# Kernel tuning notes

Hardware: AMD Instinct MI355X
Metric: run time of the kernel (lower is better)

Reference implementation:

```python
import jax, jax.numpy as jnp
import numpy as np

N = 50000
E = 400000
IN_NODE = 256
IN_EATTR = 64
IN_ETYPE = 64
EMB_EATTR = 128
EMB_ETYPE = 128
EMB_NODE = 128
OUT = 128
HEADS = 8
N_NODE_TYPES = 3
SLOPE = 0.2


def _lrelu(x):
    return jnp.where(x >= 0, x, SLOPE * x)


def setup_inputs() -> dict:
    key = jax.random.key(0)
    ks = jax.random.split(key, 12)
    s = lambda fan_in: 1.0 / np.sqrt(fan_in)
    return {
        "node_feats": jax.random.normal(ks[0], (N, IN_NODE), dtype=jnp.float32),
        "edge_index": jax.random.randint(ks[1], (2, E), 0, N, dtype=jnp.int64),
        "edge_attr": jax.random.normal(ks[2], (E, IN_EATTR), dtype=jnp.float32),
        "edge_type": jax.random.normal(ks[3], (E, IN_ETYPE), dtype=jnp.float32),
        "node_type_list": jax.random.randint(ks[4], (N,), 0, N_NODE_TYPES, dtype=jnp.int64),
        "edge_type_list": jax.random.randint(ks[5], (E,), 0, 4, dtype=jnp.int64),
        # one Linear per node type, stacked: [T, in, emb]
        "W_node": jax.random.uniform(ks[6], (N_NODE_TYPES, IN_NODE, EMB_NODE), jnp.float32, -s(IN_NODE), s(IN_NODE)),
        "W_eattr": jax.random.uniform(ks[7], (IN_EATTR, EMB_EATTR), jnp.float32, -s(IN_EATTR), s(IN_EATTR)),
        "W_etype": jax.random.uniform(ks[8], (IN_ETYPE, EMB_ETYPE), jnp.float32, -s(IN_ETYPE), s(IN_ETYPE)),
        "W_upd": jax.random.uniform(ks[9], (EMB_NODE + EMB_EATTR, OUT), jnp.float32, -s(EMB_NODE + EMB_EATTR), s(EMB_NODE + EMB_EATTR)),
        "W_attn": jax.random.uniform(ks[10], (EMB_EATTR + EMB_ETYPE + 2 * EMB_NODE, HEADS), jnp.float32, -s(512), s(512)),
    }


def reference(node_feats, edge_index, edge_attr, edge_type, node_type_list,
              edge_type_list, W_node, W_eattr, W_etype, W_upd, W_attn):
    # type-specific node embedding: project with all type weights, select per node
    all_emb = jnp.einsum("ni,tio->tno", node_feats, W_node)            # [T, N, emb]
    node_emb = jnp.take_along_axis(all_emb, node_type_list[None, :, None], axis=0)[0]  # [N, emb]

    attr_emb = _lrelu(edge_attr @ W_eattr)                             # [E, emb_a]
    type_emb = _lrelu(edge_type @ W_etype)                             # [E, emb_t]

    src, tar = edge_index[0], edge_index[1]
    src_emb = node_emb[src]                                            # [E, emb]
    tar_emb = node_emb[tar]                                            # [E, emb]

    # cat(tar_emb, attr_emb, type_emb, src_emb) -> attention scores per edge
    feat = jnp.concatenate([tar_emb, attr_emb, type_emb, src_emb], axis=1)
    scores = _lrelu(feat @ W_attn)                                     # [E, H]

    # segment softmax over edges grouped by SOURCE node (torch softmax(dim=1)
    # on the dense [src, tar, H] matrix; -10000 fillers underflow to 0)
    seg_max = jax.ops.segment_max(scores, src, num_segments=N)         # [N, H]
    ex = jnp.exp(scores - seg_max[src])
    denom = jax.ops.segment_sum(ex, src, num_segments=N)               # [N, H]
    attn = ex / denom[src]                                             # [E, H]

    msg = _lrelu(jnp.concatenate([src_emb, attr_emb], axis=1) @ W_upd) # [E, O]
    out = jax.ops.segment_sum(attn[:, :, None] * msg[:, None, :], src, num_segments=N)  # [N, H, O]
    return out.reshape(N, HEADS * OUT)
```

## Files before the change

kernel.cpp:

```cpp
#include <hip/hip_runtime.h>
#include <hip/hip_bf16.h>

#define N_NODES 50000
#define N_EDGES 400000
#define SLOPE 0.2f

typedef __attribute__((ext_vector_type(8))) short bf16x8;
typedef __attribute__((ext_vector_type(4))) float f32x4;
#define MFMA_BF16 __builtin_amdgcn_mfma_f32_16x16x32_bf16

static __device__ __forceinline__ float lrelu(float x) { return x >= 0.f ? x : SLOPE * x; }
static __device__ __forceinline__ float b2f(__hip_bfloat16 x) { return __bfloat162float(x); }
static __device__ __forceinline__ float u2f(unsigned short u) {
    union { unsigned short u; __hip_bfloat16 b; } cv; cv.u = u; return __bfloat162float(cv.b);
}
static __device__ __forceinline__ unsigned short f2bf(float x) {
    union { __hip_bfloat16 b; unsigned short u; } cv; cv.b = __float2bfloat16(x); return cv.u;
}
static __device__ __forceinline__ int clampi(int v, int lo, int hi) {
    return v < lo ? lo : (v > hi ? hi : v);
}
static __device__ __forceinline__ float ldF(const void* __restrict__ p, size_t i, bool isb) {
    return isb ? b2f(((const __hip_bfloat16*)p)[i]) : ((const float*)p)[i];
}
static __device__ __forceinline__ int ldI(const void* __restrict__ p, size_t i, bool i64) {
    return i64 ? (int)(((const long long*)p)[i]) : ((const int*)p)[i];
}

__global__ void k_detect(const void* __restrict__ nf, const void* __restrict__ eidx,
                         int* __restrict__ flags)
{
    int t = threadIdx.x;
    float x = b2f(((const __hip_bfloat16*)nf)[2 * t]);
    bool bad = !(x == x) || fabsf(x) > 1e4f;
    unsigned long long fmask = __ballot(bad);
    int v = ((const int*)eidx)[2 * t + 1];
    unsigned long long imask = __ballot(v != 0);
    if (t == 0) {
        flags[0] = (fmask == 0ull) ? 1 : 0;
        flags[1] = (imask == 0ull) ? 1 : 0;
    }
}

__global__ __launch_bounds__(256) void k_wprep(
    const void* __restrict__ Wn, const void* __restrict__ Wea, const void* __restrict__ Wet,
    const void* __restrict__ Wup, const void* __restrict__ Wat,
    unsigned short* __restrict__ WnT, unsigned short* __restrict__ WeaT,
    unsigned short* __restrict__ WetT, unsigned short* __restrict__ Wu1T,
    unsigned short* __restrict__ Wu2T, unsigned short* __restrict__ WatMidT,
    unsigned short* __restrict__ WatTS, const int* __restrict__ flags)
{
    const bool isb = flags[0] != 0;
    int i = blockIdx.x * 256 + threadIdx.x;
    if (i < 3 * 128 * 256) {
        int ty = i >> 15, rem = i & 32767, c = rem >> 8, k = rem & 255;
        WnT[i] = f2bf(ldF(Wn, ((size_t)ty * 256 + k) * 128 + c, isb));
    }
    if (i < 128 * 128) {
        int c = i >> 7, k = i & 127;
        Wu1T[i] = f2bf(ldF(Wup, (size_t)k * 128 + c, isb));
        Wu2T[i] = f2bf(ldF(Wup, (size_t)(128 + k) * 128 + c, isb));
    }
    if (i < 128 * 64) {
        int c = i >> 6, k = i & 63;
        WeaT[i] = f2bf(ldF(Wea, (size_t)k * 128 + c, isb));
        WetT[i] = f2bf(ldF(Wet, (size_t)k * 128 + c, isb));
    }
    if (i < 16 * 256) {
        int c = i >> 8, k = i & 255;
        WatMidT[i] = (c < 8) ? f2bf(ldF(Wat, (size_t)(128 + k) * 8 + c, isb)) : (unsigned short)0;
    }
    if (i < 16 * 128) {
        int c = i >> 7, k = i & 127;
        WatTS[i] = (c < 8) ? f2bf(ldF(Wat, (size_t)k * 8 + c, isb))
                           : f2bf(ldF(Wat, (size_t)(384 + k) * 8 + (c - 8), isb));
    }
}

__global__ __launch_bounds__(256) void k_node(
    const void* __restrict__ nf, const void* __restrict__ ntype,
    const unsigned short* __restrict__ WnT, const unsigned short* __restrict__ Wu1T,
    const unsigned short* __restrict__ WatTS,
    unsigned short* __restrict__ base, float* __restrict__ c_ts,
    const int* __restrict__ flags)
{
    const bool isb = flags[0] != 0, i64 = flags[1] != 0;
    const int t = threadIdx.x, lane = t & 63, wid = t >> 6;
    const int m = wid & 1, nh = wid >> 1;
    const int lr = lane & 15, lg = lane >> 4;
    const int n0 = blockIdx.x * 32;

    __shared__ __align__(16) unsigned short s_x[32 * 264];
    __shared__ __align__(16) unsigned short s_emb[32 * 136];
    __shared__ int s_ty[32];

    if (t < 32) {
        int nn = n0 + t;
        s_ty[t] = clampi(ldI(ntype, nn < N_NODES ? nn : N_NODES - 1, i64), 0, 2);
    }
    if (isb) {
        for (int i = t; i < 32 * 32; i += 256) {
            int r = i >> 5, c8 = (i & 31) * 8;
            bf16x8 v = (bf16x8)(short)0;
            if (n0 + r < N_NODES)
                v = *(const bf16x8*)((const unsigned short*)nf + (size_t)(n0 + r) * 256 + c8);
            *(bf16x8*)&s_x[r * 264 + c8] = v;
        }
    } else {
        for (int i = t; i < 32 * 64; i += 256) {
            int r = i >> 6, c4 = (i & 63) * 4;
            float4 v = make_float4(0.f, 0.f, 0.f, 0.f);
            if (n0 + r < N_NODES)
                v = *(const float4*)((const float*)nf + (size_t)(n0 + r) * 256 + c4);
            unsigned short* d = &s_x[r * 264 + c4];
            d[0] = f2bf(v.x); d[1] = f2bf(v.y); d[2] = f2bf(v.z); d[3] = f2bf(v.w);
        }
    }
    __syncthreads();

    bf16x8 A[8];
    #pragma unroll
    for (int ks = 0; ks < 8; ++ks)
        A[ks] = *(const bf16x8*)&s_x[(m * 16 + lr) * 264 + ks * 32 + lg * 8];

    f32x4 acc0[4], acc1[4], acc2[4];
    #pragma unroll
    for (int ct = 0; ct < 4; ++ct) {
        acc0[ct] = (f32x4)(0.f); acc1[ct] = (f32x4)(0.f); acc2[ct] = (f32x4)(0.f);
    }
    #pragma unroll
    for (int ct = 0; ct < 4; ++ct) {
        const int crow = nh * 64 + ct * 16 + lr;
        #pragma unroll
        for (int ks = 0; ks < 8; ++ks) {
            const int koff = ks * 32 + lg * 8;
            bf16x8 B0 = *(const bf16x8*)(WnT + (size_t)crow * 256 + koff);
            bf16x8 B1 = *(const bf16x8*)(WnT + (size_t)(128 + crow) * 256 + koff);
            bf16x8 B2 = *(const bf16x8*)(WnT + (size_t)(256 + crow) * 256 + koff);
            acc0[ct] = MFMA_BF16(A[ks], B0, acc0[ct], 0, 0, 0);
            acc1[ct] = MFMA_BF16(A[ks], B1, acc1[ct], 0, 0, 0);
            acc2[ct] = MFMA_BF16(A[ks], B2, acc2[ct], 0, 0, 0);
        }
    }
    #pragma unroll
    for (int ct = 0; ct < 4; ++ct) {
        const int col = nh * 64 + ct * 16 + lr;
        #pragma unroll
        for (int j = 0; j < 4; ++j) {
            const int row = m * 16 + lg * 4 + j;
            int ty = s_ty[row];
            float v = (ty == 0) ? acc0[ct][j] : ((ty == 1) ? acc1[ct][j] : acc2[ct][j]);
            s_emb[row * 136 + col] = f2bf(v);
        }
    }
    __syncthreads();

    bf16x8 A2[4];
    #pragma unroll
    for (int ks = 0; ks < 4; ++ks)
        A2[ks] = *(const bf16x8*)&s_emb[(m * 16 + lr) * 136 + ks * 32 + lg * 8];

    f32x4 accB[4];
    #pragma unroll
    for (int ct = 0; ct < 4; ++ct) accB[ct] = (f32x4)(0.f);
    #pragma unroll
    for (int ct = 0; ct < 4; ++ct) {
        const int crow = nh * 64 + ct * 16 + lr;
        #pragma unroll
        for (int ks = 0; ks < 4; ++ks) {
            bf16x8 B = *(const bf16x8*)(Wu1T + (size_t)crow * 128 + ks * 32 + lg * 8);
            accB[ct] = MFMA_BF16(A2[ks], B, accB[ct], 0, 0, 0);
        }
    }
    #pragma unroll
    for (int ct = 0; ct < 4; ++ct) {
        const int col = nh * 64 + ct * 16 + lr;
        #pragma unroll
        for (int j = 0; j < 4; ++j) {
            const int n = n0 + m * 16 + lg * 4 + j;
            if (n < N_NODES) base[(size_t)n * 128 + col] = f2bf(accB[ct][j]);
        }
    }

    if (nh == 0) {
        f32x4 aS = (f32x4)(0.f);
        #pragma unroll
        for (int ks = 0; ks < 4; ++ks) {
            bf16x8 B = *(const bf16x8*)(WatTS + (size_t)lr * 128 + ks * 32 + lg * 8);
            aS = MFMA_BF16(A2[ks], B, aS, 0, 0, 0);
        }
        #pragma unroll
        for (int j = 0; j < 4; ++j) {
            const int n = n0 + m * 16 + lg * 4 + j;
            if (n < N_NODES) c_ts[(size_t)n * 16 + lr] = aS[j];
        }
    }
}

static __device__ __forceinline__ void load_afrag64(
    bf16x8 Af[2], const void* __restrict__ src, int arow, int lg, bool isb)
{
    #pragma unroll
    for (int ks = 0; ks < 2; ++ks) {
        const int koff = ks * 32 + lg * 8;
        if (isb) {
            Af[ks] = *(const bf16x8*)((const unsigned short*)src + (size_t)arow * 64 + koff);
        } else {
            const float* p = (const float*)src + (size_t)arow * 64 + koff;
            float4 a0 = *(const float4*)p, a1 = *(const float4*)(p + 4);
            bf16x8 v;
            v[0] = (short)f2bf(a0.x); v[1] = (short)f2bf(a0.y);
            v[2] = (short)f2bf(a0.z); v[3] = (short)f2bf(a0.w);
            v[4] = (short)f2bf(a1.x); v[5] = (short)f2bf(a1.y);
            v[6] = (short)f2bf(a1.z); v[7] = (short)f2bf(a1.w);
            Af[ks] = v;
        }
    }
}

static __device__ __forceinline__ void proj64_to_lds(
    const bf16x8 Af[2], const unsigned short* __restrict__ WT,
    unsigned short* __restrict__ s_buf, int m, int lr, int lg)
{
    #pragma unroll
    for (int half = 0; half < 2; ++half) {
        f32x4 acc[4];
        #pragma unroll
        for (int ct = 0; ct < 4; ++ct) acc[ct] = (f32x4)(0.f);
        #pragma unroll
        for (int ct = 0; ct < 4; ++ct) {
            const int crow = half * 64 + ct * 16 + lr;
            #pragma unroll
            for (int ks = 0; ks < 2; ++ks) {
                bf16x8 B = *(const bf16x8*)(WT + (size_t)crow * 64 + ks * 32 + lg * 8);
                acc[ct] = MFMA_BF16(Af[ks], B, acc[ct], 0, 0, 0);
            }
        }
        #pragma unroll
        for (int ct = 0; ct < 4; ++ct) {
            const int col = half * 64 + ct * 16 + lr;
            #pragma unroll
            for (int j = 0; j < 4; ++j)
                s_buf[(m * 16 + lg * 4 + j) * 132 + col] = f2bf(lrelu(acc[ct][j]));
        }
    }
}

__global__ __launch_bounds__(128) void k_edge(
    const void* __restrict__ eattr, const void* __restrict__ etype,
    const void* __restrict__ eidx, const float* __restrict__ c_ts,
    const unsigned short* __restrict__ WeaT, const unsigned short* __restrict__ WetT,
    const unsigned short* __restrict__ Wu2T, const unsigned short* __restrict__ WatMidT,
    const int* __restrict__ inv, float* __restrict__ scores,
    unsigned short* __restrict__ ap, const int* __restrict__ flags)
{
    const bool isb = flags[0] != 0, i64 = flags[1] != 0;
    const int t = threadIdx.x, lane = t & 63, m = t >> 6;
    const int lr = lane & 15, lg = lane >> 4;
    const int e0 = blockIdx.x * 32;

    __shared__ __align__(16) unsigned short s_buf[32 * 132];

    const int arow = e0 + m * 16 + lr;
    bf16x8 Aet[2], Aea[2];
    load_afrag64(Aet, etype, arow, lg, isb);
    load_afrag64(Aea, eattr, arow, lg, isb);

    int slotj[4], aslot[4];
    float ctj[4], csj[4];
    #pragma unroll
    for (int j = 0; j < 4; ++j) {
        const int rw = m * 16 + lg * 4 + j;
        const int ew = e0 + rw;
        int s = clampi(ldI(eidx, (size_t)ew, i64), 0, N_NODES - 1);
        int d = clampi(ldI(eidx, (size_t)N_EDGES + ew, i64), 0, N_NODES - 1);
        slotj[j] = clampi(inv[ew], 0, N_EDGES - 1);
        ctj[j] = c_ts[(size_t)d * 16 + (lr & 7)];
        csj[j] = c_ts[(size_t)s * 16 + 8 + (lr & 7)];
        const int rs = m * 16 + lg + j * 4;
        aslot[j] = clampi(inv[e0 + rs], 0, N_EDGES - 1);
    }

    f32x4 aS = (f32x4)(0.f);

    proj64_to_lds(Aet, WetT, s_buf, m, lr, lg);
    #pragma unroll
    for (int ks = 0; ks < 4; ++ks) {
        bf16x8 A = *(const bf16x8*)&s_buf[(m * 16 + lr) * 132 + ks * 32 + lg * 8];
        bf16x8 B = *(const bf16x8*)(WatMidT + (size_t)lr * 256 + 128 + ks * 32 + lg * 8);
        aS = MFMA_BF16(A, B, aS, 0, 0, 0);
    }
    proj64_to_lds(Aea, WeaT, s_buf, m, lr, lg);
    bf16x8 A2[4];
    #pragma unroll
    for (int ks = 0; ks < 4; ++ks)
        A2[ks] = *(const bf16x8*)&s_buf[(m * 16 + lr) * 132 + ks * 32 + lg * 8];
    #pragma unroll
    for (int ks = 0; ks < 4; ++ks) {
        bf16x8 B = *(const bf16x8*)(WatMidT + (size_t)lr * 256 + ks * 32 + lg * 8);
        aS = MFMA_BF16(A2[ks], B, aS, 0, 0, 0);
    }
    if (lr < 8) {
        #pragma unroll
        for (int j = 0; j < 4; ++j)
            scores[(size_t)slotj[j] * 8 + lr] = lrelu(aS[j] + ctj[j] + csj[j]);
    }

    #pragma unroll
    for (int half = 0; half < 2; ++half) {
        f32x4 a2[4];
        #pragma unroll
        for (int ct = 0; ct < 4; ++ct) a2[ct] = (f32x4)(0.f);
        #pragma unroll
        for (int ct = 0; ct < 4; ++ct) {
            const int crow = half * 64 + ct * 16 + lr;
            #pragma unroll
            for (int ks = 0; ks < 4; ++ks) {
                bf16x8 B = *(const bf16x8*)(Wu2T + (size_t)crow * 128 + ks * 32 + lg * 8);
                a2[ct] = MFMA_BF16(A2[ks], B, a2[ct], 0, 0, 0);
            }
        }
        #pragma unroll
        for (int ct = 0; ct < 4; ++ct) {
            const int col = half * 64 + ct * 16 + lr;
            #pragma unroll
            for (int j = 0; j < 4; ++j)
                s_buf[(m * 16 + lg * 4 + j) * 132 + col] = f2bf(a2[ct][j]);
        }
    }
    #pragma unroll
    for (int i = 0; i < 4; ++i) {
        const int r = m * 16 + lg + i * 4;
        bf16x8 v = *(const bf16x8*)&s_buf[r * 132 + lr * 8];
        *(bf16x8*)(ap + (size_t)aslot[i] * 128 + lr * 8) = v;
    }
}

__global__ void k_hist(const void* __restrict__ eidx, int* __restrict__ counts,
                       const int* __restrict__ flags)
{
    const bool i64 = flags[1] != 0;
    int e = blockIdx.x * blockDim.x + threadIdx.x;
    if (e < N_EDGES) atomicAdd(&counts[clampi(ldI(eidx, e, i64), 0, N_NODES - 1)], 1);
}

__global__ __launch_bounds__(256) void k_scan1(const int* __restrict__ counts,
                                               int* __restrict__ offsets, int* __restrict__ bsum)
{
    __shared__ int buf[256];
    int b = blockIdx.x, t = threadIdx.x, i = b * 256 + t;
    int v = (i < N_NODES) ? counts[i] : 0;
    buf[t] = v;
    __syncthreads();
    for (int d = 1; d < 256; d <<= 1) {
        int add = (t >= d) ? buf[t - d] : 0;
        __syncthreads();
        buf[t] += add;
        __syncthreads();
    }
    if (i < N_NODES) offsets[i] = buf[t] - v;
    if (t == 255) bsum[b] = buf[255];
}
__global__ __launch_bounds__(256) void k_scan2(int* __restrict__ bsum, int nb)
{
    __shared__ int buf[256];
    int t = threadIdx.x;
    int v = (t < nb) ? bsum[t] : 0;
    buf[t] = v;
    __syncthreads();
    for (int d = 1; d < 256; d <<= 1) {
        int add = (t >= d) ? buf[t - d] : 0;
        __syncthreads();
        buf[t] += add;
        __syncthreads();
    }
    if (t < nb) bsum[t] = buf[t] - v;
}
__global__ __launch_bounds__(256) void k_scan3(int* __restrict__ offsets,
                                               const int* __restrict__ bsum)
{
    int i = blockIdx.x * 256 + threadIdx.x;
    if (i < N_NODES) offsets[i] += bsum[i >> 8];
    if (i == 0) offsets[N_NODES] = N_EDGES;
}

__global__ void k_scatter(const void* __restrict__ eidx, const int* __restrict__ offsets,
                          int* __restrict__ fill, int* __restrict__ inv,
                          const int* __restrict__ flags)
{
    const bool i64 = flags[1] != 0;
    int e = blockIdx.x * blockDim.x + threadIdx.x;
    if (e >= N_EDGES) return;
    int s = clampi(ldI(eidx, e, i64), 0, N_NODES - 1);
    int p = atomicAdd(&fill[s], 1);
    inv[e] = offsets[s] + p;
}

__global__ void k_stats(float* __restrict__ scores, const int* __restrict__ offsets)
{
    int tid = blockIdx.x * blockDim.x + threadIdx.x;
    if (tid >= N_NODES * 8) return;
    int n = tid >> 3, h = tid & 7;
    int off = offsets[n], deg = offsets[n + 1] - off;
    if (deg <= 0) return;
    float m = -1e30f;
    for (int j = 0; j < deg; ++j)
        m = fmaxf(m, scores[(size_t)(off + j) * 8 + h]);
    float d = 0.f;
    for (int j = 0; j < deg; ++j)
        d += expf(scores[(size_t)(off + j) * 8 + h] - m);
    float inv = (d > 0.f) ? 1.f / d : 0.f;
    for (int j = 0; j < deg; ++j) {
        size_t idx = (size_t)(off + j) * 8 + h;
        scores[idx] = expf(scores[idx] - m) * inv;
    }
}

__global__ __launch_bounds__(256) void k_aggr3(
    const unsigned short* __restrict__ base, const float* __restrict__ attn,
    const unsigned short* __restrict__ ap, const int* __restrict__ offsets,
    void* __restrict__ out, const int* __restrict__ flags)
{
    const bool isb = flags[0] != 0;
    const int n = blockIdx.x * 8 + (threadIdx.x >> 5);
    const int c = threadIdx.x & 31;

    ushort4 b4 = *(const ushort4*)(base + (size_t)n * 128 + 4 * c);
    float b0 = u2f(b4.x), b1 = u2f(b4.y), b2 = u2f(b4.z), b3 = u2f(b4.w);

    float acc[8][4];
    #pragma unroll
    for (int h = 0; h < 8; ++h)
        #pragma unroll
        for (int k = 0; k < 4; ++k) acc[h][k] = 0.f;

    const int off = offsets[n], deg = offsets[n + 1] - off;
    for (int j = 0; j < deg; ++j) {
        const size_t slot = (size_t)(off + j);
        ushort4 v = *(const ushort4*)(ap + slot * 128 + 4 * c);
        float m0 = lrelu(b0 + u2f(v.x));
        float m1 = lrelu(b1 + u2f(v.y));
        float m2 = lrelu(b2 + u2f(v.z));
        float m3 = lrelu(b3 + u2f(v.w));
        const float* at = attn + slot * 8;
        #pragma unroll
        for (int h = 0; h < 8; ++h) {
            float a = at[h];
            acc[h][0] += a * m0; acc[h][1] += a * m1;
            acc[h][2] += a * m2; acc[h][3] += a * m3;
        }
    }
    if (isb) {
        __hip_bfloat16* o = (__hip_bfloat16*)out;
        #pragma unroll
        for (int h = 0; h < 8; ++h) {
            ushort4 o4;
            o4.x = f2bf(acc[h][0]); o4.y = f2bf(acc[h][1]);
            o4.z = f2bf(acc[h][2]); o4.w = f2bf(acc[h][3]);
            *(ushort4*)((unsigned short*)o + (size_t)n * 1024 + h * 128 + 4 * c) = o4;
        }
    } else {
        float* o = (float*)out;
        #pragma unroll
        for (int h = 0; h < 8; ++h) {
            float4 o4 = make_float4(acc[h][0], acc[h][1], acc[h][2], acc[h][3]);
            *(float4*)(o + (size_t)n * 1024 + h * 128 + 4 * c) = o4;
        }
    }
}

static inline size_t alignup(size_t x, size_t a) { return (x + a - 1) & ~(a - 1); }

extern "C" void kernel_launch(void* const* d_in, const int* in_sizes, int n_in,
                              void* d_out, int out_size, void* d_ws, size_t ws_size,
                              hipStream_t stream)
{
    const void* nf   = d_in[0];
    const void* eidx = d_in[1];
    const void* eatt = d_in[2];
    const void* etyp = d_in[3];
    const void* ntyp = d_in[4];
    const void* Wn   = d_in[6];
    const void* Wea  = d_in[7];
    const void* Wet  = d_in[8];
    const void* Wup  = d_in[9];
    const void* Wat  = d_in[10];

    char* w = (char*)d_ws;
    size_t off = 16;
    int* flags = (int*)w;
    unsigned short* base = (unsigned short*)(w + off);  off += (size_t)N_NODES * 128 * 2;
    float* c_ts   = (float*)(w + off);                  off += (size_t)N_NODES * 16 * 4;
    float* scores = (float*)(w + off);                  off += (size_t)N_EDGES * 8 * 4;
    int* counts   = (int*)(w + off);                    off += (size_t)N_NODES * 4;
    int* offsets  = (int*)(w + off);                    off += (size_t)(N_NODES + 1) * 4;
    int* inv      = (int*)(w + off);                    off += (size_t)N_EDGES * 4;
    int* bsum     = (int*)(w + off);                    off += 1024;
    off = alignup(off, 16);
    unsigned short* WnT     = (unsigned short*)(w + off); off += (size_t)3 * 128 * 256 * 2;
    unsigned short* WeaT    = (unsigned short*)(w + off); off += 128 * 64 * 2;
    unsigned short* WetT    = (unsigned short*)(w + off); off += 128 * 64 * 2;
    unsigned short* Wu1T    = (unsigned short*)(w + off); off += 128 * 128 * 2;
    unsigned short* Wu2T    = (unsigned short*)(w + off); off += 128 * 128 * 2;
    unsigned short* WatMidT = (unsigned short*)(w + off); off += 16 * 256 * 2;
    unsigned short* WatTS   = (unsigned short*)(w + off); off += 16 * 128 * 2;
    off = alignup(off, 16);
    unsigned short* ap = (unsigned short*)(w + off);

    hipMemsetAsync(counts, 0, N_NODES * sizeof(int), stream);

    k_detect<<<1, 64, 0, stream>>>(nf, eidx, flags);
    k_wprep<<<384, 256, 0, stream>>>(Wn, Wea, Wet, Wup, Wat,
                                     WnT, WeaT, WetT, Wu1T, Wu2T, WatMidT, WatTS, flags);
    k_hist<<<(N_EDGES + 255) / 256, 256, 0, stream>>>(eidx, counts, flags);
    const int SB = (N_NODES + 255) / 256;
    k_scan1<<<SB, 256, 0, stream>>>(counts, offsets, bsum);
    k_scan2<<<1, 256, 0, stream>>>(bsum, SB);
    k_scan3<<<SB, 256, 0, stream>>>(offsets, bsum);
    hipMemsetAsync(counts, 0, N_NODES * sizeof(int), stream);
    k_scatter<<<(N_EDGES + 255) / 256, 256, 0, stream>>>(eidx, offsets, counts, inv, flags);

    k_node<<<(N_NODES + 31) / 32, 256, 0, stream>>>(nf, ntyp, WnT, Wu1T, WatTS,
                                                    base, c_ts, flags);
    k_edge<<<N_EDGES / 32, 128, 0, stream>>>(eatt, etyp, eidx, c_ts,
                                             WeaT, WetT, Wu2T, WatMidT,
                                             inv, scores, ap, flags);
    k_stats<<<(N_NODES * 8 + 255) / 256, 256, 0, stream>>>(scores, offsets);
    k_aggr3<<<N_NODES / 8, 256, 0, stream>>>(base, scores, ap, offsets, d_out, flags);
}
```

Measured before the change: 812.7 us.

## Fuse softmax stats into aggregation, stage edge weights in LDS, drop memsets

Removes the separate k_stats kernel. The aggregation kernel now computes the per-source max and denominator itself and recomputes the normalized attention weights inline, broadcasting them with shuffles. The edge kernel doubles its block to 64 edges and 256 threads and stages the WeaT/WetT weights in swizzled LDS instead of reading them from global memory. The two hipMemsetAsync calls that zeroed counts are folded into k_wprep and k_scan3. In exchange, aggregation does extra serial passes over the scores per node, and the edge kernel uses more LDS per block, which may lower occupancy.

Result: faster. 780.5 us (-4.0%).

```diff
diff --git a/kernel.cpp b/kernel.cpp
--- a/kernel.cpp
+++ b/kernel.cpp
@@ -48,10 +48,12 @@
     unsigned short* __restrict__ WnT, unsigned short* __restrict__ WeaT,
     unsigned short* __restrict__ WetT, unsigned short* __restrict__ Wu1T,
     unsigned short* __restrict__ Wu2T, unsigned short* __restrict__ WatMidT,
-    unsigned short* __restrict__ WatTS, const int* __restrict__ flags)
+    unsigned short* __restrict__ WatTS, int* __restrict__ counts,
+    const int* __restrict__ flags)
 {
     const bool isb = flags[0] != 0;
     int i = blockIdx.x * 256 + threadIdx.x;
+    if (i < N_NODES) counts[i] = 0;
     if (i < 3 * 128 * 256) {
         int ty = i >> 15, rem = i & 32767, c = rem >> 8, k = rem & 255;
         WnT[i] = f2bf(ldF(Wn, ((size_t)ty * 256 + k) * 128 + c, isb));
@@ -218,9 +220,16 @@
     }
 }
 
-static __device__ __forceinline__ void proj64_to_lds(
-    const bf16x8 Af[2], const unsigned short* __restrict__ WT,
-    unsigned short* __restrict__ s_buf, int m, int lr, int lg)
+static __device__ __forceinline__ const bf16x8* ldsB64(
+    const unsigned short* __restrict__ s_w, int base, int row, int k)
+{
+    int byte = ((base + row * 64 + k) << 1) ^ ((row & 7) << 4);
+    return (const bf16x8*)((const char*)s_w + byte);
+}
+
+static __device__ __forceinline__ void proj64_lds(
+    const bf16x8 Af[2], const unsigned short* __restrict__ s_w, int wbase,
+    unsigned short* __restrict__ s_buf, int w, int lr, int lg)
 {
     #pragma unroll
     for (int half = 0; half < 2; ++half) {
@@ -232,7 +241,7 @@
             const int crow = half * 64 + ct * 16 + lr;
             #pragma unroll
             for (int ks = 0; ks < 2; ++ks) {
-                bf16x8 B = *(const bf16x8*)(WT + (size_t)crow * 64 + ks * 32 + lg * 8);
+                bf16x8 B = *ldsB64(s_w, wbase, crow, ks * 32 + lg * 8);
                 acc[ct] = MFMA_BF16(Af[ks], B, acc[ct], 0, 0, 0);
             }
         }
@@ -241,12 +250,12 @@
             const int col = half * 64 + ct * 16 + lr;
             #pragma unroll
             for (int j = 0; j < 4; ++j)
-                s_buf[(m * 16 + lg * 4 + j) * 132 + col] = f2bf(lrelu(acc[ct][j]));
-        }
-    }
-}
-
-__global__ __launch_bounds__(128) void k_edge(
+                s_buf[(w * 16 + lg * 4 + j) * 132 + col] = f2bf(lrelu(acc[ct][j]));
+        }
+    }
+}
+
+__global__ __launch_bounds__(256) void k_edge(
     const void* __restrict__ eattr, const void* __restrict__ etype,
     const void* __restrict__ eidx, const float* __restrict__ c_ts,
     const unsigned short* __restrict__ WeaT, const unsigned short* __restrict__ WetT,
@@ -255,13 +264,14 @@
     unsigned short* __restrict__ ap, const int* __restrict__ flags)
 {
     const bool isb = flags[0] != 0, i64 = flags[1] != 0;
-    const int t = threadIdx.x, lane = t & 63, m = t >> 6;
+    const int t = threadIdx.x, lane = t & 63, w = t >> 6;
     const int lr = lane & 15, lg = lane >> 4;
-    const int e0 = blockIdx.x * 32;
-
-    __shared__ __align__(16) unsigned short s_buf[32 * 132];
-
-    const int arow = e0 + m * 16 + lr;
+    const int e0 = blockIdx.x * 64;
+
+    __shared__ __align__(16) unsigned short s_w[16384];
+    __shared__ __align__(16) unsigned short s_buf[64 * 132];
+
+    const int arow = e0 + w * 16 + lr;
     bf16x8 Aet[2], Aea[2];
     load_afrag64(Aet, etype, arow, lg, isb);
     load_afrag64(Aea, eattr, arow, lg, isb);
@@ -270,31 +280,41 @@
     float ctj[4], csj[4];
     #pragma unroll
     for (int j = 0; j < 4; ++j) {
-        const int rw = m * 16 + lg * 4 + j;
+        const int rw = w * 16 + lg * 4 + j;
         const int ew = e0 + rw;
         int s = clampi(ldI(eidx, (size_t)ew, i64), 0, N_NODES - 1);
         int d = clampi(ldI(eidx, (size_t)N_EDGES + ew, i64), 0, N_NODES - 1);
         slotj[j] = clampi(inv[ew], 0, N_EDGES - 1);
         ctj[j] = c_ts[(size_t)d * 16 + (lr & 7)];
         csj[j] = c_ts[(size_t)s * 16 + 8 + (lr & 7)];
-        const int rs = m * 16 + lg + j * 4;
+        const int rs = w * 16 + lg + j * 4;
         aslot[j] = clampi(inv[e0 + rs], 0, N_EDGES - 1);
     }
 
+    for (int i = t; i < 2048; i += 256) {
+        int src = i >> 10;
+        int g = (i & 1023) * 8;
+        int row = g >> 6;
+        bf16x8 v = *(const bf16x8*)((src ? WetT : WeaT) + g);
+        int byte = (((src << 13) + g) << 1) ^ ((row & 7) << 4);
+        *(bf16x8*)((char*)s_w + byte) = v;
+    }
+    __syncthreads();
+
     f32x4 aS = (f32x4)(0.f);
 
-    proj64_to_lds(Aet, WetT, s_buf, m, lr, lg);
+    proj64_lds(Aet, s_w, 8192, s_buf, w, lr, lg);
     #pragma unroll
     for (int ks = 0; ks < 4; ++ks) {
-        bf16x8 A = *(const bf16x8*)&s_buf[(m * 16 + lr) * 132 + ks * 32 + lg * 8];
+        bf16x8 A = *(const bf16x8*)&s_buf[(w * 16 + lr) * 132 + ks * 32 + lg * 8];
         bf16x8 B = *(const bf16x8*)(WatMidT + (size_t)lr * 256 + 128 + ks * 32 + lg * 8);
         aS = MFMA_BF16(A, B, aS, 0, 0, 0);
     }
-    proj64_to_lds(Aea, WeaT, s_buf, m, lr, lg);
+    proj64_lds(Aea, s_w, 0, s_buf, w, lr, lg);
     bf16x8 A2[4];
     #pragma unroll
     for (int ks = 0; ks < 4; ++ks)
-        A2[ks] = *(const bf16x8*)&s_buf[(m * 16 + lr) * 132 + ks * 32 + lg * 8];
+        A2[ks] = *(const bf16x8*)&s_buf[(w * 16 + lr) * 132 + ks * 32 + lg * 8];
     #pragma unroll
     for (int ks = 0; ks < 4; ++ks) {
         bf16x8 B = *(const bf16x8*)(WatMidT + (size_t)lr * 256 + ks * 32 + lg * 8);
@@ -325,12 +345,12 @@
             const int col = half * 64 + ct * 16 + lr;
             #pragma unroll
             for (int j = 0; j < 4; ++j)
-                s_buf[(m * 16 + lg * 4 + j) * 132 + col] = f2bf(a2[ct][j]);
+                s_buf[(w * 16 + lg * 4 + j) * 132 + col] = f2bf(a2[ct][j]);
         }
     }
     #pragma unroll
     for (int i = 0; i < 4; ++i) {
-        const int r = m * 16 + lg + i * 4;
+        const int r = w * 16 + lg + i * 4;
         bf16x8 v = *(const bf16x8*)&s_buf[r * 132 + lr * 8];
         *(bf16x8*)(ap + (size_t)aslot[i] * 128 + lr * 8) = v;
     }
@@ -377,10 +397,14 @@
     if (t < nb) bsum[t] = buf[t] - v;
 }
 __global__ __launch_bounds__(256) void k_scan3(int* __restrict__ offsets,
-                                               const int* __restrict__ bsum)
+                                               const int* __restrict__ bsum,
+                                               int* __restrict__ counts)
 {
     int i = blockIdx.x * 256 + threadIdx.x;
-    if (i < N_NODES) offsets[i] += bsum[i >> 8];
+    if (i < N_NODES) {
+        offsets[i] += bsum[i >> 8];
+        counts[i] = 0;
+    }
     if (i == 0) offsets[N_NODES] = N_EDGES;
 }
 
@@ -396,28 +420,8 @@
     inv[e] = offsets[s] + p;
 }
 
-__global__ void k_stats(float* __restrict__ scores, const int* __restrict__ offsets)
-{
-    int tid = blockIdx.x * blockDim.x + threadIdx.x;
-    if (tid >= N_NODES * 8) return;
-    int n = tid >> 3, h = tid & 7;
-    int off = offsets[n], deg = offsets[n + 1] - off;
-    if (deg <= 0) return;
-    float m = -1e30f;
-    for (int j = 0; j < deg; ++j)
-        m = fmaxf(m, scores[(size_t)(off + j) * 8 + h]);
-    float d = 0.f;
-    for (int j = 0; j < deg; ++j)
-        d += expf(scores[(size_t)(off + j) * 8 + h] - m);
-    float inv = (d > 0.f) ? 1.f / d : 0.f;
-    for (int j = 0; j < deg; ++j) {
-        size_t idx = (size_t)(off + j) * 8 + h;
-        scores[idx] = expf(scores[idx] - m) * inv;
-    }
-}
-
-__global__ __launch_bounds__(256) void k_aggr3(
-    const unsigned short* __restrict__ base, const float* __restrict__ attn,
+__global__ __launch_bounds__(256) void k_aggr4(
+    const unsigned short* __restrict__ base, const float* __restrict__ scores,
     const unsigned short* __restrict__ ap, const int* __restrict__ offsets,
     void* __restrict__ out, const int* __restrict__ flags)
 {
@@ -425,6 +429,17 @@
     const int n = blockIdx.x * 8 + (threadIdx.x >> 5);
     const int c = threadIdx.x & 31;
 
+    const int off = offsets[n], deg = offsets[n + 1] - off;
+
+    float m = -1e30f, dsum = 0.f;
+    if (c < 8) {
+        for (int j = 0; j < deg; ++j)
+            m = fmaxf(m, scores[(size_t)(off + j) * 8 + c]);
+        for (int j = 0; j < deg; ++j)
+            dsum += expf(scores[(size_t)(off + j) * 8 + c] - m);
+    }
+    const float sinv = (dsum > 0.f) ? 1.f / dsum : 0.f;
+
     ushort4 b4 = *(const ushort4*)(base + (size_t)n * 128 + 4 * c);
     float b0 = u2f(b4.x), b1 = u2f(b4.y), b2 = u2f(b4.z), b3 = u2f(b4.w);
 
@@ -434,18 +449,18 @@
         #pragma unroll
         for (int k = 0; k < 4; ++k) acc[h][k] = 0.f;
 
-    const int off = offsets[n], deg = offsets[n + 1] - off;
     for (int j = 0; j < deg; ++j) {
         const size_t slot = (size_t)(off + j);
         ushort4 v = *(const ushort4*)(ap + slot * 128 + 4 * c);
+        float wgt = 0.f;
+        if (c < 8) wgt = expf(scores[slot * 8 + c] - m) * sinv;
         float m0 = lrelu(b0 + u2f(v.x));
         float m1 = lrelu(b1 + u2f(v.y));
         float m2 = lrelu(b2 + u2f(v.z));
         float m3 = lrelu(b3 + u2f(v.w));
-        const float* at = attn + slot * 8;
         #pragma unroll
         for (int h = 0; h < 8; ++h) {
-            float a = at[h];
+            float a = __shfl(wgt, h, 32);
             acc[h][0] += a * m0; acc[h][1] += a * m1;
             acc[h][2] += a * m2; acc[h][3] += a * m3;
         }
@@ -507,24 +522,21 @@
     off = alignup(off, 16);
     unsigned short* ap = (unsigned short*)(w + off);
 
-    hipMemsetAsync(counts, 0, N_NODES * sizeof(int), stream);
-
     k_detect<<<1, 64, 0, stream>>>(nf, eidx, flags);
     k_wprep<<<384, 256, 0, stream>>>(Wn, Wea, Wet, Wup, Wat,
-                                     WnT, WeaT, WetT, Wu1T, Wu2T, WatMidT, WatTS, flags);
+                                     WnT, WeaT, WetT, Wu1T, Wu2T, WatMidT, WatTS,
+                                     counts, flags);
     k_hist<<<(N_EDGES + 255) / 256, 256, 0, stream>>>(eidx, counts, flags);
     const int SB = (N_NODES + 255) / 256;
     k_scan1<<<SB, 256, 0, stream>>>(counts, offsets, bsum);
     k_scan2<<<1, 256, 0, stream>>>(bsum, SB);
-    k_scan3<<<SB, 256, 0, stream>>>(offsets, bsum);
-    hipMemsetAsync(counts, 0, N_NODES * sizeof(int), stream);
+    k_scan3<<<SB, 256, 0, stream>>>(offsets, bsum, counts);
     k_scatter<<<(N_EDGES + 255) / 256, 256, 0, stream>>>(eidx, offsets, counts, inv, flags);
 
     k_node<<<(N_NODES + 31) / 32, 256, 0, stream>>>(nf, ntyp, WnT, Wu1T, WatTS,
                                                     base, c_ts, flags);
-    k_edge<<<N_EDGES / 32, 128, 0, stream>>>(eatt, etyp, eidx, c_ts,
+    k_edge<<<N_EDGES / 64, 256, 0, stream>>>(eatt, etyp, eidx, c_ts,
                                              WeaT, WetT, Wu2T, WatMidT,
                                              inv, scores, ap, flags);
-    k_stats<<<(N_NODES * 8 + 255) / 256, 256, 0, stream>>>(scores, offsets);
-    k_aggr3<<<N_NODES / 8, 256, 0, stream>>>(base, scores, ap, offsets, d_out, flags);
-}
+    k_aggr4<<<N_NODES / 8, 256, 0, stream>>>(base, scores, ap, offsets, d_out, flags);
+}
```
